# Kernel tuning notes

Hardware: AMD Instinct MI355X
Metric: run time of the kernel (lower is better)

## Reference

```python
import jax, jax.numpy as jnp
import numpy as np

N = 50000          # nodes
E = 800000         # edges (avg degree 16)
DIN = 128          # d_input
H = 8              # heads per layer
D = 16             # per-head hidden dim
HID = H * D        # 128
ALPHA = 0.2        # LeakyReLU negative slope in GAT attention
BN_EPS = 1e-5


def _xavier(key, shape):
    fan_in, fan_out = shape[0], shape[-1]
    lim = np.sqrt(6.0 / (fan_in + fan_out)).astype(np.float32)
    return jax.random.uniform(key, shape, jnp.float32, -lim, lim)


def setup_inputs() -> dict:
    key = jax.random.key(0)
    ks = jax.random.split(key, 8)
    x = jax.random.normal(ks[0], (N, DIN), jnp.float32)
    edge_idx = jax.random.randint(ks[1], (2, E), 0, N)
    W1 = _xavier(ks[2], (DIN, HID))
    a1 = _xavier(ks[3], (H, 2 * D))
    W2 = _xavier(ks[4], (HID, HID))
    a2 = _xavier(ks[5], (H, 2 * D))
    W3 = _xavier(ks[6], (HID, HID))
    a3 = _xavier(ks[7], (H, 2 * D))
    ones = jnp.ones((HID,), jnp.float32)
    zeros = jnp.zeros((HID,), jnp.float32)
    return {"x": x, "edge_idx": edge_idx,
            "W1": W1, "a1": a1, "W2": W2, "a2": a2, "W3": W3, "a3": a3,
            "g1": ones, "b1": zeros, "g2": ones, "b2": zeros, "g3": ones, "b3": zeros}


def _leaky(x):
    return jnp.where(x >= 0, x, ALPHA * x)


def _gat_layer(x, src, dst, W, a):
    # x: [N, Fin]; W: [Fin, H*D]; a: [H, 2D]
    h = (x @ W).reshape(-1, H, D)                       # [N, H, D]
    e_src = jnp.einsum('nhd,hd->nh', h, a[:, :D])       # a^T part for source node
    e_dst = jnp.einsum('nhd,hd->nh', h, a[:, D:])       # a^T part for destination node
    e = _leaky(e_src[src] + e_dst[dst])                 # [E, H]
    m = jax.ops.segment_max(e, dst, num_segments=N)     # per-dst stable softmax max
    m = jnp.where(jnp.isfinite(m), m, 0.0)              # empty segments -> 0
    w = jnp.exp(e - m[dst])                             # [E, H]
    den = jax.ops.segment_sum(w, dst, num_segments=N)   # [N, H]
    agg = jax.ops.segment_sum(h[src] * w[:, :, None], dst, num_segments=N)  # [N, H, D]
    out = agg / (den[:, :, None] + 1e-16)
    return out.reshape(-1, HID)                         # concat heads


def _bn(x, g, b):
    # BatchNorm1d training-mode math over the node axis
    mu = x.mean(axis=0)
    var = x.var(axis=0)
    return g * (x - mu) * jax.lax.rsqrt(var + BN_EPS) + b


def reference(x, edge_idx, W1, a1, W2, a2, W3, a3, g1, b1, g2, b2, g3, b3):
    src, dst = edge_idx[0], edge_idx[1]
    h1 = jax.nn.elu(_bn(_gat_layer(x, src, dst, W1, a1), g1, b1))
    h2 = jax.nn.elu(_bn(_gat_layer(h1, src, dst, W2, a2), g2, b2))
    h3_in = h1 + h2  # skip connection
    return _bn(_gat_layer(h3_in, src, dst, W3, a3), g3, b3)
```

## Files before the change

### kernel.cpp

```cpp
#include <hip/hip_runtime.h>
#include <hip/hip_bf16.h>
#include <hip/hip_fp16.h>
#include <cstddef>

#define NNODES 50000
#define NEDGES 800000
#define HID 128
#define NHEAD 8
#define AGG_NB (NNODES / 16)
#define NSLICE 64
#define SLAYER (NSLICE * 512)

#define NBUCK 196
#define BCH 2048
#define BIN_NB ((NEDGES + BCH - 1) / BCH)

typedef __attribute__((ext_vector_type(4))) float floatx4;
typedef _Float16 __attribute__((ext_vector_type(8))) half8;
typedef _Float16 __attribute__((ext_vector_type(2))) half2v;

static inline size_t align_up(size_t x, size_t a) { return (x + a - 1) & ~(a - 1); }

__device__ inline float fexp2(float x) {
#if __has_builtin(__builtin_amdgcn_exp2f)
    return __builtin_amdgcn_exp2f(x);
#else
    return __expf(x * 0.69314718055994531f);
#endif
}

__device__ inline unsigned short f2h(float f) {
    return __builtin_bit_cast(unsigned short, (_Float16)f);
}

__global__ __launch_bounds__(256) void init_kernel(const float* __restrict__ W1,
                                                   const float* __restrict__ W2,
                                                   const float* __restrict__ W3,
                                                   unsigned short* __restrict__ Wt,
                                                   int* __restrict__ zeroA, int nA,
                                                   float* __restrict__ zeroB, int nB) {
    int b = blockIdx.x;
    int t = threadIdx.x;
    if (b < 192) {
        int layer = b >> 6;
        const float* W = (layer == 0) ? W1 : ((layer == 1) ? W2 : W3);
        int idx = (b & 63) * 256 + t;
        int n = idx & 127;
        int k = idx >> 7;
        Wt[layer * 16384 + n * 128 + k] = f2h(W[idx]);
    } else {
        int nb = gridDim.x - 192;
        int bb = b - 192;
        for (int i = bb * 256 + t; i < nA; i += nb * 256) zeroA[i] = 0;
        for (int i = bb * 256 + t; i < nB; i += nb * 256) zeroB[i] = 0.f;
    }
}

__global__ __launch_bounds__(256) void bin_count_kernel(const int* __restrict__ edge,
                                                        int* __restrict__ bucketCnt) {
    __shared__ int h[NBUCK];
    int t = threadIdx.x;
    if (t < NBUCK) h[t] = 0;
    __syncthreads();
    for (int i = blockIdx.x * 256 + t; i < NEDGES; i += gridDim.x * 256)
        atomicAdd(&h[edge[NEDGES + i] >> 8], 1);
    __syncthreads();
    if (t < NBUCK && h[t]) atomicAdd(&bucketCnt[t], h[t]);
}

__global__ __launch_bounds__(256) void bucket_scan_kernel(const int* __restrict__ bucketCnt,
                                                          int* __restrict__ bucketBase) {
    __shared__ int sA[256];
    int t = threadIdx.x;
    int v = (t < NBUCK) ? bucketCnt[t] : 0;
    sA[t] = v;
    __syncthreads();
    for (int off = 1; off < 256; off <<= 1) {
        int x = (t >= off) ? sA[t - off] : 0;
        __syncthreads();
        sA[t] += x;
        __syncthreads();
    }
    if (t < NBUCK) bucketBase[t] = sA[t] - v;
    if (t == 0) bucketBase[NBUCK] = NEDGES;
}

__global__ __launch_bounds__(256) void bin_scatter_kernel(const int* __restrict__ edge,
                                                          const int* __restrict__ bucketBase,
                                                          int* __restrict__ bucketCursor,
                                                          unsigned int* __restrict__ binned) {
    __shared__ int sA[256];
    __shared__ int hcnt[NBUCK];
    __shared__ int hbase[NBUCK];
    __shared__ int gbase[NBUCK];
    __shared__ unsigned int sEnt[BCH];
    __shared__ unsigned char sBk[BCH];
    int t = threadIdx.x;
    int e0 = blockIdx.x * BCH;
    int nv = NEDGES - e0;
    if (nv > BCH) nv = BCH;

    if (t < NBUCK) hcnt[t] = 0;
    __syncthreads();

    int myB[8];
    int myR[8];
    unsigned int myP[8];
    #pragma unroll
    for (int j = 0; j < 8; ++j) {
        int idx = j * 256 + t;
        myB[j] = -1;
        if (idx < nv) {
            int s = edge[e0 + idx];
            int d = edge[NEDGES + e0 + idx];
            int bk = d >> 8;
            myB[j] = bk;
            myP[j] = (unsigned)s | ((unsigned)(d & 255) << 16);
            myR[j] = atomicAdd(&hcnt[bk], 1);
        }
    }
    __syncthreads();
    int hc = (t < NBUCK) ? hcnt[t] : 0;
    sA[t] = hc;
    __syncthreads();
    for (int off = 1; off < 256; off <<= 1) {
        int x = (t >= off) ? sA[t - off] : 0;
        __syncthreads();
        sA[t] += x;
        __syncthreads();
    }
    if (t < NBUCK) {
        hbase[t] = sA[t] - hc;
        gbase[t] = bucketBase[t] + atomicAdd(&bucketCursor[t], hc);
    }
    __syncthreads();
    #pragma unroll
    for (int j = 0; j < 8; ++j) {
        if (myB[j] >= 0) {
            int p = hbase[myB[j]] + myR[j];
            sEnt[p] = myP[j];
            sBk[p] = (unsigned char)myB[j];
        }
    }
    __syncthreads();
    #pragma unroll
    for (int j = 0; j < 8; ++j) {
        int i = j * 256 + t;
        if (i < nv) {
            int bk = sBk[i];
            binned[gbase[bk] + (i - hbase[bk])] = sEnt[i];
        }
    }
}

__global__ __launch_bounds__(256) void fine_csr_kernel(const int* __restrict__ bucketCnt,
                                                       const int* __restrict__ bucketBase,
                                                       const unsigned int* __restrict__ binned,
                                                       int* __restrict__ offs,
                                                       int* __restrict__ csr) {
    __shared__ int sA[256];
    __shared__ int sB[256];
    int t = threadIdx.x;
    int b = blockIdx.x;
    int cntb = bucketCnt[b];
    int base = bucketBase[b];
    sB[t] = 0;
    __syncthreads();
    for (int i = t; i < cntb; i += 256)
        atomicAdd(&sB[(binned[base + i] >> 16) & 255], 1);
    __syncthreads();
    int nc = sB[t];
    sA[t] = nc;
    __syncthreads();
    for (int off = 1; off < 256; off <<= 1) {
        int x = (t >= off) ? sA[t - off] : 0;
        __syncthreads();
        sA[t] += x;
        __syncthreads();
    }
    int nodeBase = base + sA[t] - nc;
    int gid = b * 256 + t;
    if (gid < NNODES) offs[gid] = nodeBase;
    if (b == NBUCK - 1 && t == 0) offs[NNODES] = NEDGES;
    sB[t] = nodeBase;
    __syncthreads();
    for (int i = t; i < cntb; i += 256) {
        unsigned e = binned[base + i];
        int pos = atomicAdd(&sB[(e >> 16) & 255], 1);
        csr[pos] = (int)(e & 0xFFFFu);
    }
}

__global__ __launch_bounds__(256) void bn_finalize_kernel(const float* __restrict__ statsPart,
                                                          const float* __restrict__ g,
                                                          const float* __restrict__ b,
                                                          float* __restrict__ ssv) {
    __shared__ float sm[256];
    int t = threadIdx.x;
    const float* base = statsPart + (t & 127) + ((t >> 7) << 7);
    float s = 0.f;
    #pragma unroll 8
    for (int k = 0; k < NSLICE; ++k) s += base[k * 512];
    sm[t] = s;
    __syncthreads();
    if (t < 128) {
        float mu = sm[t] / (float)NNODES;
        float var = sm[128 + t] / (float)NNODES - mu * mu;
        float rstd = rsqrtf(var + 1e-5f);
        float scale = g[t] * rstd;
        ssv[t] = scale;
        ssv[128 + t] = b[t] - mu * scale;
    }
}

#define GROWS 64
#define ASTRIDE 136
#define LOG2E 1.4426950408889634f
__global__ __launch_bounds__(256, 4) void gemm_kernel(const float* __restrict__ Xin,
                                                      const float* __restrict__ skip,
                                                      const float* __restrict__ ssv,
                                                      const unsigned short* __restrict__ Wt,
                                                      const float* __restrict__ a,
                                                      float* __restrict__ Hw,
                                                      unsigned short* __restrict__ Hb,
                                                      float* __restrict__ esrc,
                                                      float* __restrict__ edst,
                                                      int mode) {
    __shared__ unsigned short As[GROWS * ASTRIDE];
    int tid = threadIdx.x;
    int rowBase = blockIdx.x * GROWS;

    int r = tid >> 2;
    int cs = (tid & 3) * 32;
    int gr = rowBase + r;
    bool valid = gr < NNODES;
    float4 vv[8];
    if (valid) {
        #pragma unroll
        for (int j = 0; j < 8; ++j)
            vv[j] = *(const float4*)(Xin + (size_t)gr * HID + cs + j * 4);
    } else {
        #pragma unroll
        for (int j = 0; j < 8; ++j) vv[j] = make_float4(0.f, 0.f, 0.f, 0.f);
    }

    if (mode >= 1 && valid) {
        #pragma unroll
        for (int j = 0; j < 8; ++j) {
            int ch = cs + j * 4;
            float4 sc = *(const float4*)(ssv + ch);
            float4 sh = *(const float4*)(ssv + 128 + ch);
            float4 v = vv[j];
            v.x = sc.x * v.x + sh.x;
            v.y = sc.y * v.y + sh.y;
            v.z = sc.z * v.z + sh.z;
            v.w = sc.w * v.w + sh.w;
            v.x = (v.x > 0.f) ? v.x : expm1f(v.x);
            v.y = (v.y > 0.f) ? v.y : expm1f(v.y);
            v.z = (v.z > 0.f) ? v.z : expm1f(v.z);
            v.w = (v.w > 0.f) ? v.w : expm1f(v.w);
            if (mode == 2) {
                float4 s = *(const float4*)(skip + (size_t)gr * HID + ch);
                v.x += s.x; v.y += s.y; v.z += s.z; v.w += s.w;
            }
            vv[j] = v;
        }
        if (mode == 1) {
            #pragma unroll
            for (int j = 0; j < 8; ++j)
                *(float4*)(Hw + (size_t)gr * HID + cs + j * 4) = vv[j];
        }
    }
    {
        unsigned int pk[16];
        #pragma unroll
        for (int j = 0; j < 8; ++j) {
            pk[2 * j]     = __builtin_bit_cast(unsigned int,
                                __builtin_amdgcn_cvt_pkrtz(vv[j].x, vv[j].y));
            pk[2 * j + 1] = __builtin_bit_cast(unsigned int,
                                __builtin_amdgcn_cvt_pkrtz(vv[j].z, vv[j].w));
        }
        #pragma unroll
        for (int q = 0; q < 4; ++q)
            *(uint4*)(&As[r * ASTRIDE + cs + q * 8]) =
                make_uint4(pk[4 * q], pk[4 * q + 1], pk[4 * q + 2], pk[4 * q + 3]);
    }

    int wv = tid >> 6;
    int lane = tid & 63;
    int l15 = lane & 15;
    int quad = lane >> 4;
    const unsigned short* Arow = &As[(wv * 16 + l15) * ASTRIDE + quad * 8];
    half8 af[4];
    #pragma unroll
    for (int c = 0; c < 4; ++c) af[c] = *(const half8*)(Arow + c * 32);

    floatx4 acc[8];
    #pragma unroll
    for (int h = 0; h < 8; ++h) {
        acc[h] = (floatx4){0.f, 0.f, 0.f, 0.f};
        const unsigned short* Brow = Wt + (h * 16 + l15) * 128 + quad * 8;
        #pragma unroll
        for (int c = 0; c < 4; ++c) {
            half8 bfr = *(const half8*)(Brow + c * 32);
            acc[h] = __builtin_amdgcn_mfma_f32_16x16x32_f16(af[c], bfr, acc[h], 0, 0, 0);
        }
    }

    #pragma unroll
    for (int h = 0; h < 8; ++h) {
        #pragma unroll
        for (int reg = 0; reg < 4; ++reg)
            As[(wv * 16 + quad * 4 + reg) * ASTRIDE + h * 16 + l15] = f2h(acc[h][reg]);
    }

    {
        int rr = tid >> 2;
        int hp = tid & 3;
        int grr = rowBase + rr;
        const unsigned short* row = &As[rr * ASTRIDE + hp * 32];
        uint4 u[4];
        #pragma unroll
        for (int q = 0; q < 4; ++q) u[q] = *(const uint4*)(row + q * 8);
        if (grr < NNODES) {
            uint4* dst = (uint4*)(Hb + (size_t)grr * HID + hp * 32);
            #pragma unroll
            for (int q = 0; q < 4; ++q) dst[q] = u[q];
            float f[32];
            #pragma unroll
            for (int q = 0; q < 4; ++q) {
                unsigned int* pu = (unsigned int*)&u[q];
                #pragma unroll
                for (int j = 0; j < 4; ++j) {
                    half2v hv = __builtin_bit_cast(half2v, pu[j]);
                    f[q * 8 + 2 * j]     = (float)hv[0];
                    f[q * 8 + 2 * j + 1] = (float)hv[1];
                }
            }
            int h0 = hp * 2, h1 = hp * 2 + 1;
            float es0 = 0.f, ev0 = 0.f, es1 = 0.f, ev1 = 0.f;
            #pragma unroll
            for (int j = 0; j < 16; ++j) {
                es0 += f[j] * a[h0 * 32 + j];
                ev0 += f[j] * a[h0 * 32 + 16 + j];
                es1 += f[16 + j] * a[h1 * 32 + j];
                ev1 += f[16 + j] * a[h1 * 32 + 16 + j];
            }
            esrc[grr * NHEAD + h0] = es0 * LOG2E;
            esrc[grr * NHEAD + h1] = es1 * LOG2E;
            edst[grr * NHEAD + h0] = ev0 * LOG2E;
            edst[grr * NHEAD + h1] = ev1 * LOG2E;
        }
    }
}

__global__ __launch_bounds__(256) void aggregate_kernel(const int* __restrict__ offs,
                                                        const int* __restrict__ csr,
                                                        const float* __restrict__ esrc,
                                                        const float* __restrict__ edst,
                                                        const unsigned int* __restrict__ Hb,
                                                        float* __restrict__ out,
                                                        float* __restrict__ statsPart) {
    int tid = threadIdx.x;
    int wv = tid >> 6;
    int lane = tid & 63;
    int grp = lane >> 4;
    int sub = lane & 15;
    int head = sub >> 1;
    int n = blockIdx.x * 16 + wv * 4 + grp;
    int beg = offs[n], end = offs[n + 1];
    float ed = edst[n * NHEAD + head];
    float acc[8];
    #pragma unroll
    for (int q = 0; q < 8; ++q) acc[q] = 0.f;
    float den = 0.f;
    for (int i = beg; i < end; i += 4) {
        int ss[4];
        #pragma unroll
        for (int j = 0; j < 4; ++j)
            ss[j] = csr[min(i + j, end - 1)];
        float ee[4];
        uint4 hh[4];
        #pragma unroll
        for (int j = 0; j < 4; ++j)
            ee[j] = esrc[(unsigned)ss[j] * 8u + (unsigned)head];
        #pragma unroll
        for (int j = 0; j < 4; ++j)
            hh[j] = *(const uint4*)(Hb + (unsigned)ss[j] * 64u + (unsigned)sub * 4u);
        #pragma unroll
        for (int j = 0; j < 4; ++j) {
            float e = ee[j] + ed;
            e = fmaxf(e, 0.2f * e);
            float w = fexp2(e);
            w = (i + j < end) ? w : 0.f;
            den += w;
            half2v h0 = __builtin_bit_cast(half2v, hh[j].x);
            half2v h1 = __builtin_bit_cast(half2v, hh[j].y);
            half2v h2 = __builtin_bit_cast(half2v, hh[j].z);
            half2v h3 = __builtin_bit_cast(half2v, hh[j].w);
            acc[0] += w * (float)h0[0];
            acc[1] += w * (float)h0[1];
            acc[2] += w * (float)h1[0];
            acc[3] += w * (float)h1[1];
            acc[4] += w * (float)h2[0];
            acc[5] += w * (float)h2[1];
            acc[6] += w * (float)h3[0];
            acc[7] += w * (float)h3[1];
        }
    }
    float inv = 1.f / (den + 1e-16f);
    float4 o0 = make_float4(acc[0] * inv, acc[1] * inv, acc[2] * inv, acc[3] * inv);
    float4 o1 = make_float4(acc[4] * inv, acc[5] * inv, acc[6] * inv, acc[7] * inv);
    float* orow = out + (size_t)n * HID + sub * 8;
    *(float4*)orow = o0;
    *(float4*)(orow + 4) = o1;

    __shared__ float sm[16 * 136];
    float* srow = &sm[(wv * 4 + grp) * 136 + sub * 8];
    *(float4*)srow = o0;
    *(float4*)(srow + 4) = o1;
    __syncthreads();
    if (tid < 128) {
        float s = 0.f, s2 = 0.f;
        #pragma unroll
        for (int rr = 0; rr < 16; ++rr) {
            float v = sm[rr * 136 + tid];
            s += v;
            s2 += v * v;
        }
        float* slice = statsPart + (blockIdx.x & (NSLICE - 1)) * 512;
        atomicAdd(&slice[tid], s);
        atomicAdd(&slice[128 + tid], s2);
    }
}

__global__ __launch_bounds__(256) void final_apply_kernel(const float* __restrict__ X,
                                                          const float* __restrict__ ssv,
                                                          float* __restrict__ out) {
    __shared__ float ssm[256];
    int tid = threadIdx.x;
    ssm[tid] = ssv[tid];
    __syncthreads();
    int total4 = NNODES * HID / 4;
    for (int i = blockIdx.x * 256 + tid; i < total4; i += gridDim.x * 256) {
        float4 v = ((const float4*)X)[i];
        int c4 = (i & 31) * 4;
        float4 sc = *(const float4*)(ssm + c4);
        float4 sh = *(const float4*)(ssm + 128 + c4);
        v.x = sc.x * v.x + sh.x;
        v.y = sc.y * v.y + sh.y;
        v.z = sc.z * v.z + sh.z;
        v.w = sc.w * v.w + sh.w;
        ((float4*)out)[i] = v;
    }
}

extern "C" void kernel_launch(void* const* d_in, const int* in_sizes, int n_in,
                              void* d_out, int out_size, void* d_ws, size_t ws_size,
                              hipStream_t stream) {
    const float* x   = (const float*)d_in[0];
    const int* edge  = (const int*)d_in[1];
    const float* W1  = (const float*)d_in[2];
    const float* a1  = (const float*)d_in[3];
    const float* W2  = (const float*)d_in[4];
    const float* a2  = (const float*)d_in[5];
    const float* W3  = (const float*)d_in[6];
    const float* a3  = (const float*)d_in[7];
    const float* g1  = (const float*)d_in[8];
    const float* b1  = (const float*)d_in[9];
    const float* g2  = (const float*)d_in[10];
    const float* b2  = (const float*)d_in[11];
    const float* g3  = (const float*)d_in[12];
    const float* b3  = (const float*)d_in[13];
    float* outp      = (float*)d_out;

    char* p = (char*)d_ws;
    size_t cur = 0;
    auto carve = [&](size_t bytes) {
        void* r = p + cur;
        cur = align_up(cur + bytes, 256);
        return r;
    };
    int*   offs   = (int*)carve((NNODES + 1) * sizeof(int));
    int*   csr    = (int*)carve(NEDGES * sizeof(int));
    unsigned short* wt = (unsigned short*)carve(3 * 16384 * sizeof(unsigned short));
    unsigned short* hb = (unsigned short*)carve((size_t)NNODES * HID * sizeof(unsigned short));
    float* agg    = (float*)carve((size_t)NNODES * HID * sizeof(float));
    float* h1     = (float*)carve((size_t)NNODES * HID * sizeof(float));
    float* esrc   = (float*)carve((size_t)NNODES * NHEAD * sizeof(float));
    float* edst   = (float*)carve((size_t)NNODES * NHEAD * sizeof(float));
    float* stats  = (float*)carve(3 * SLAYER * sizeof(float));
    int*   bcnt   = (int*)carve((3 * NBUCK + 1) * sizeof(int));
    int*   bcur   = bcnt + NBUCK;
    int*   bbase  = bcnt + 2 * NBUCK;
    float* ssv    = (float*)carve(3 * 256 * sizeof(float));
    float* stats1 = stats;
    float* stats2 = stats + SLAYER;
    float* stats3 = stats + 2 * SLAYER;
    float* ssv1 = ssv;
    float* ssv2 = ssv + 256;
    float* ssv3 = ssv + 512;
    unsigned int* binned = (unsigned int*)h1;

    const int GB = (NNODES + GROWS - 1) / GROWS;

    init_kernel<<<256, 256, 0, stream>>>(W1, W2, W3, wt,
                                         bcnt, 2 * NBUCK,
                                         stats, 3 * SLAYER);
    bin_count_kernel<<<256, 256, 0, stream>>>(edge, bcnt);
    bucket_scan_kernel<<<1, 256, 0, stream>>>(bcnt, bbase);
    bin_scatter_kernel<<<BIN_NB, 256, 0, stream>>>(edge, bbase, bcur, binned);
    fine_csr_kernel<<<NBUCK, 256, 0, stream>>>(bcnt, bbase, binned, offs, csr);

    gemm_kernel<<<GB, 256, 0, stream>>>(x, nullptr, nullptr,
                                        wt, a1, nullptr, hb, esrc, edst, 0);
    aggregate_kernel<<<AGG_NB, 256, 0, stream>>>(offs, csr, esrc, edst,
                                                 (const unsigned int*)hb, agg, stats1);
    bn_finalize_kernel<<<1, 256, 0, stream>>>(stats1, g1, b1, ssv1);

    gemm_kernel<<<GB, 256, 0, stream>>>(agg, nullptr, ssv1,
                                        wt + 16384, a2, h1, hb, esrc, edst, 1);
    aggregate_kernel<<<AGG_NB, 256, 0, stream>>>(offs, csr, esrc, edst,
                                                 (const unsigned int*)hb, agg, stats2);
    bn_finalize_kernel<<<1, 256, 0, stream>>>(stats2, g2, b2, ssv2);

    gemm_kernel<<<GB, 256, 0, stream>>>(agg, h1, ssv2,
                                        wt + 32768, a3, nullptr, hb, esrc, edst, 2);
    aggregate_kernel<<<AGG_NB, 256, 0, stream>>>(offs, csr, esrc, edst,
                                                 (const unsigned int*)hb, agg, stats3);
    bn_finalize_kernel<<<1, 256, 0, stream>>>(stats3, g3, b3, ssv3);

    final_apply_kernel<<<768, 256, 0, stream>>>(agg, ssv3, outp);
}
```

Baseline: 407.1 us.

## Load GEMM A fragments directly from global and split head columns across waves

After: 395.2 us. 1.03x faster.

```diff
diff --git a/kernel.cpp b/kernel.cpp
--- a/kernel.cpp
+++ b/kernel.cpp
@@ -213,8 +213,8 @@
     }
 }
 
-#define GROWS 64
-#define ASTRIDE 136
+#define GROWS 32
+#define TSTRIDE 76
 #define LOG2E 1.4426950408889634f
 __global__ __launch_bounds__(256, 4) void gemm_kernel(const float* __restrict__ Xin,
                                                       const float* __restrict__ skip,
@@ -226,130 +226,150 @@
                                                       float* __restrict__ esrc,
                                                       float* __restrict__ edst,
                                                       int mode) {
-    __shared__ unsigned short As[GROWS * ASTRIDE];
+    __shared__ unsigned short As[4 * 16 * TSTRIDE];
     int tid = threadIdx.x;
-    int rowBase = blockIdx.x * GROWS;
-
-    int r = tid >> 2;
-    int cs = (tid & 3) * 32;
-    int gr = rowBase + r;
-    bool valid = gr < NNODES;
-    float4 vv[8];
-    if (valid) {
-        #pragma unroll
-        for (int j = 0; j < 8; ++j)
-            vv[j] = *(const float4*)(Xin + (size_t)gr * HID + cs + j * 4);
-    } else {
-        #pragma unroll
-        for (int j = 0; j < 8; ++j) vv[j] = make_float4(0.f, 0.f, 0.f, 0.f);
-    }
-
-    if (mode >= 1 && valid) {
-        #pragma unroll
-        for (int j = 0; j < 8; ++j) {
-            int ch = cs + j * 4;
-            float4 sc = *(const float4*)(ssv + ch);
-            float4 sh = *(const float4*)(ssv + 128 + ch);
-            float4 v = vv[j];
-            v.x = sc.x * v.x + sh.x;
-            v.y = sc.y * v.y + sh.y;
-            v.z = sc.z * v.z + sh.z;
-            v.w = sc.w * v.w + sh.w;
-            v.x = (v.x > 0.f) ? v.x : expm1f(v.x);
-            v.y = (v.y > 0.f) ? v.y : expm1f(v.y);
-            v.z = (v.z > 0.f) ? v.z : expm1f(v.z);
-            v.w = (v.w > 0.f) ? v.w : expm1f(v.w);
-            if (mode == 2) {
-                float4 s = *(const float4*)(skip + (size_t)gr * HID + ch);
-                v.x += s.x; v.y += s.y; v.z += s.z; v.w += s.w;
-            }
-            vv[j] = v;
-        }
-        if (mode == 1) {
-            #pragma unroll
-            for (int j = 0; j < 8; ++j)
-                *(float4*)(Hw + (size_t)gr * HID + cs + j * 4) = vv[j];
-        }
-    }
-    {
-        unsigned int pk[16];
-        #pragma unroll
-        for (int j = 0; j < 8; ++j) {
-            pk[2 * j]     = __builtin_bit_cast(unsigned int,
-                                __builtin_amdgcn_cvt_pkrtz(vv[j].x, vv[j].y));
-            pk[2 * j + 1] = __builtin_bit_cast(unsigned int,
-                                __builtin_amdgcn_cvt_pkrtz(vv[j].z, vv[j].w));
-        }
-        #pragma unroll
-        for (int q = 0; q < 4; ++q)
-            *(uint4*)(&As[r * ASTRIDE + cs + q * 8]) =
-                make_uint4(pk[4 * q], pk[4 * q + 1], pk[4 * q + 2], pk[4 * q + 3]);
-    }
-
     int wv = tid >> 6;
     int lane = tid & 63;
     int l15 = lane & 15;
     int quad = lane >> 4;
-    const unsigned short* Arow = &As[(wv * 16 + l15) * ASTRIDE + quad * 8];
+    int whalf = wv & 1;
+    int rowBase = blockIdx.x * GROWS + (wv >> 1) * 16;
+    int gr = rowBase + l15;
+    bool valid = gr < NNODES;
+
+    float4 va[8];
+    if (valid) {
+        const float* xr = Xin + (size_t)gr * HID + quad * 8;
+        #pragma unroll
+        for (int c = 0; c < 4; ++c) {
+            va[2 * c]     = *(const float4*)(xr + c * 32);
+            va[2 * c + 1] = *(const float4*)(xr + c * 32 + 4);
+        }
+    } else {
+        #pragma unroll
+        for (int j = 0; j < 8; ++j) va[j] = make_float4(0.f, 0.f, 0.f, 0.f);
+    }
+    float4 vs[8];
+    if (mode == 2 && valid) {
+        const float* sr = skip + (size_t)gr * HID + quad * 8;
+        #pragma unroll
+        for (int c = 0; c < 4; ++c) {
+            vs[2 * c]     = *(const float4*)(sr + c * 32);
+            vs[2 * c + 1] = *(const float4*)(sr + c * 32 + 4);
+        }
+    }
+
+    half8 bf[2][4];
+    {
+        const unsigned short* wb = Wt + ((whalf * 4) * 16 + l15) * 128 + quad * 8;
+        #pragma unroll
+        for (int c = 0; c < 4; ++c) bf[0][c] = *(const half8*)(wb + c * 32);
+    }
+
+    if (mode >= 1 && valid) {
+        #pragma unroll
+        for (int c = 0; c < 4; ++c) {
+            #pragma unroll
+            for (int hh = 0; hh < 2; ++hh) {
+                int ch = quad * 8 + c * 32 + hh * 4;
+                float4 sc = *(const float4*)(ssv + ch);
+                float4 sh = *(const float4*)(ssv + 128 + ch);
+                float4 v = va[2 * c + hh];
+                v.x = sc.x * v.x + sh.x;
+                v.y = sc.y * v.y + sh.y;
+                v.z = sc.z * v.z + sh.z;
+                v.w = sc.w * v.w + sh.w;
+                v.x = (v.x > 0.f) ? v.x : expm1f(v.x);
+                v.y = (v.y > 0.f) ? v.y : expm1f(v.y);
+                v.z = (v.z > 0.f) ? v.z : expm1f(v.z);
+                v.w = (v.w > 0.f) ? v.w : expm1f(v.w);
+                if (mode == 2) {
+                    float4 s = vs[2 * c + hh];
+                    v.x += s.x; v.y += s.y; v.z += s.z; v.w += s.w;
+                }
+                va[2 * c + hh] = v;
+            }
+        }
+        if (mode == 1 && whalf == 0) {
+            float* hw = Hw + (size_t)gr * HID + quad * 8;
+            #pragma unroll
+            for (int c = 0; c < 4; ++c) {
+                *(float4*)(hw + c * 32)     = va[2 * c];
+                *(float4*)(hw + c * 32 + 4) = va[2 * c + 1];
+            }
+        }
+    }
     half8 af[4];
     #pragma unroll
-    for (int c = 0; c < 4; ++c) af[c] = *(const half8*)(Arow + c * 32);
-
-    floatx4 acc[8];
-    #pragma unroll
-    for (int h = 0; h < 8; ++h) {
-        acc[h] = (floatx4){0.f, 0.f, 0.f, 0.f};
-        const unsigned short* Brow = Wt + (h * 16 + l15) * 128 + quad * 8;
-        #pragma unroll
-        for (int c = 0; c < 4; ++c) {
-            half8 bfr = *(const half8*)(Brow + c * 32);
-            acc[h] = __builtin_amdgcn_mfma_f32_16x16x32_f16(af[c], bfr, acc[h], 0, 0, 0);
-        }
-    }
-
-    #pragma unroll
-    for (int h = 0; h < 8; ++h) {
+    for (int c = 0; c < 4; ++c) {
+        uint4 pk;
+        pk.x = __builtin_bit_cast(unsigned int, __builtin_amdgcn_cvt_pkrtz(va[2*c].x,   va[2*c].y));
+        pk.y = __builtin_bit_cast(unsigned int, __builtin_amdgcn_cvt_pkrtz(va[2*c].z,   va[2*c].w));
+        pk.z = __builtin_bit_cast(unsigned int, __builtin_amdgcn_cvt_pkrtz(va[2*c+1].x, va[2*c+1].y));
+        pk.w = __builtin_bit_cast(unsigned int, __builtin_amdgcn_cvt_pkrtz(va[2*c+1].z, va[2*c+1].w));
+        af[c] = __builtin_bit_cast(half8, pk);
+    }
+
+    floatx4 acc[4];
+    #pragma unroll
+    for (int hb = 0; hb < 4; ++hb) {
+        if (hb < 3) {
+            const unsigned short* wn = Wt + ((whalf * 4 + hb + 1) * 16 + l15) * 128 + quad * 8;
+            #pragma unroll
+            for (int c = 0; c < 4; ++c) bf[(hb + 1) & 1][c] = *(const half8*)(wn + c * 32);
+        }
+        acc[hb] = (floatx4){0.f, 0.f, 0.f, 0.f};
+        #pragma unroll
+        for (int c = 0; c < 4; ++c)
+            acc[hb] = __builtin_amdgcn_mfma_f32_16x16x32_f16(af[c], bf[hb & 1][c], acc[hb], 0, 0, 0);
+    }
+
+    unsigned short* ws = &As[wv * 16 * TSTRIDE];
+    #pragma unroll
+    for (int hb = 0; hb < 4; ++hb) {
         #pragma unroll
         for (int reg = 0; reg < 4; ++reg)
-            As[(wv * 16 + quad * 4 + reg) * ASTRIDE + h * 16 + l15] = f2h(acc[h][reg]);
+            ws[(quad * 4 + reg) * TSTRIDE + hb * 16 + l15] = f2h(acc[hb][reg]);
     }
 
     {
-        int rr = tid >> 2;
-        int hp = tid & 3;
-        int grr = rowBase + rr;
-        const unsigned short* row = &As[rr * ASTRIDE + hp * 32];
-        uint4 u[4];
-        #pragma unroll
-        for (int q = 0; q < 4; ++q) u[q] = *(const uint4*)(row + q * 8);
-        if (grr < NNODES) {
-            uint4* dst = (uint4*)(Hb + (size_t)grr * HID + hp * 32);
-            #pragma unroll
-            for (int q = 0; q < 4; ++q) dst[q] = u[q];
-            float f[32];
-            #pragma unroll
-            for (int q = 0; q < 4; ++q) {
-                unsigned int* pu = (unsigned int*)&u[q];
+        int rloc = lane >> 2;
+        int cpart = lane & 3;
+        int grow = rowBase + rloc;
+        const unsigned short* rrow = &ws[rloc * TSTRIDE + cpart * 16];
+        uint4 u0 = *(const uint4*)(rrow);
+        uint4 u1 = *(const uint4*)(rrow + 8);
+        if (grow < NNODES) {
+            int chb = whalf * 64 + cpart * 16;
+            uint4* dst = (uint4*)(Hb + (size_t)grow * HID + chb);
+            dst[0] = u0;
+            dst[1] = u1;
+            float f[16];
+            {
+                unsigned int* pu = (unsigned int*)&u0;
                 #pragma unroll
                 for (int j = 0; j < 4; ++j) {
                     half2v hv = __builtin_bit_cast(half2v, pu[j]);
-                    f[q * 8 + 2 * j]     = (float)hv[0];
-                    f[q * 8 + 2 * j + 1] = (float)hv[1];
+                    f[2 * j]     = (float)hv[0];
+                    f[2 * j + 1] = (float)hv[1];
+                }
+                pu = (unsigned int*)&u1;
+                #pragma unroll
+                for (int j = 0; j < 4; ++j) {
+                    half2v hv = __builtin_bit_cast(half2v, pu[j]);
+                    f[8 + 2 * j]     = (float)hv[0];
+                    f[8 + 2 * j + 1] = (float)hv[1];
                 }
             }
-            int h0 = hp * 2, h1 = hp * 2 + 1;
-            float es0 = 0.f, ev0 = 0.f, es1 = 0.f, ev1 = 0.f;
+            int head = whalf * 4 + cpart;
+            float es = 0.f, ev = 0.f;
             #pragma unroll
             for (int j = 0; j < 16; ++j) {
-                es0 += f[j] * a[h0 * 32 + j];
-                ev0 += f[j] * a[h0 * 32 + 16 + j];
-                es1 += f[16 + j] * a[h1 * 32 + j];
-                ev1 += f[16 + j] * a[h1 * 32 + 16 + j];
+                es += f[j] * a[head * 32 + j];
+                ev += f[j] * a[head * 32 + 16 + j];
             }
-            esrc[grr * NHEAD + h0] = es0 * LOG2E;
-            esrc[grr * NHEAD + h1] = es1 * LOG2E;
-            edst[grr * NHEAD + h0] = ev0 * LOG2E;
-            edst[grr * NHEAD + h1] = ev1 * LOG2E;
+            esrc[grow * NHEAD + head] = es * LOG2E;
+            edst[grow * NHEAD + head] = ev * LOG2E;
         }
     }
 }
```

## Stage GEMM weights in LDS and keep the h1 skip activation in fp16

Applied to the files above, without the earlier changes.

Measured after the change: 373.4 us. 1.09x faster.

```diff
diff --git a/kernel.cpp b/kernel.cpp
--- a/kernel.cpp
+++ b/kernel.cpp
@@ -216,19 +216,27 @@
 #define GROWS 64
 #define ASTRIDE 136
 #define LOG2E 1.4426950408889634f
-__global__ __launch_bounds__(256, 4) void gemm_kernel(const float* __restrict__ Xin,
-                                                      const float* __restrict__ skip,
-                                                      const float* __restrict__ ssv,
-                                                      const unsigned short* __restrict__ Wt,
-                                                      const float* __restrict__ a,
-                                                      float* __restrict__ Hw,
-                                                      unsigned short* __restrict__ Hb,
-                                                      float* __restrict__ esrc,
-                                                      float* __restrict__ edst,
-                                                      int mode) {
+__global__ __launch_bounds__(256) void gemm_kernel(const float* __restrict__ Xin,
+                                                   const unsigned short* __restrict__ skip16,
+                                                   const float* __restrict__ ssv,
+                                                   const unsigned short* __restrict__ Wt,
+                                                   const float* __restrict__ a,
+                                                   unsigned short* __restrict__ Hw16,
+                                                   unsigned short* __restrict__ Hb,
+                                                   float* __restrict__ esrc,
+                                                   float* __restrict__ edst,
+                                                   int mode) {
     __shared__ unsigned short As[GROWS * ASTRIDE];
+    __shared__ unsigned short Bs[128 * ASTRIDE];
     int tid = threadIdx.x;
     int rowBase = blockIdx.x * GROWS;
+
+    uint4 breg[8];
+    #pragma unroll
+    for (int q = 0; q < 8; ++q) {
+        int i = q * 256 + tid;
+        breg[q] = *(const uint4*)(Wt + (i >> 4) * 128 + (i & 15) * 8);
+    }
 
     int r = tid >> 2;
     int cs = (tid & 3) * 32;
@@ -244,7 +252,19 @@
         for (int j = 0; j < 8; ++j) vv[j] = make_float4(0.f, 0.f, 0.f, 0.f);
     }
 
+    #pragma unroll
+    for (int q = 0; q < 8; ++q) {
+        int i = q * 256 + tid;
+        *(uint4*)(&Bs[(i >> 4) * ASTRIDE + (i & 15) * 8]) = breg[q];
+    }
+
     if (mode >= 1 && valid) {
+        uint4 sk[4];
+        if (mode == 2) {
+            #pragma unroll
+            for (int q = 0; q < 4; ++q)
+                sk[q] = *(const uint4*)(skip16 + (size_t)gr * HID + cs + q * 8);
+        }
         #pragma unroll
         for (int j = 0; j < 8; ++j) {
             int ch = cs + j * 4;
@@ -260,15 +280,15 @@
             v.z = (v.z > 0.f) ? v.z : expm1f(v.z);
             v.w = (v.w > 0.f) ? v.w : expm1f(v.w);
             if (mode == 2) {
-                float4 s = *(const float4*)(skip + (size_t)gr * HID + ch);
-                v.x += s.x; v.y += s.y; v.z += s.z; v.w += s.w;
+                const unsigned int* pu = (const unsigned int*)&sk[j >> 1];
+                half2v s0 = __builtin_bit_cast(half2v, pu[(j & 1) * 2]);
+                half2v s1 = __builtin_bit_cast(half2v, pu[(j & 1) * 2 + 1]);
+                v.x += (float)s0[0];
+                v.y += (float)s0[1];
+                v.z += (float)s1[0];
+                v.w += (float)s1[1];
             }
             vv[j] = v;
-        }
-        if (mode == 1) {
-            #pragma unroll
-            for (int j = 0; j < 8; ++j)
-                *(float4*)(Hw + (size_t)gr * HID + cs + j * 4) = vv[j];
         }
     }
     {
@@ -280,11 +300,19 @@
             pk[2 * j + 1] = __builtin_bit_cast(unsigned int,
                                 __builtin_amdgcn_cvt_pkrtz(vv[j].z, vv[j].w));
         }
+        if (mode == 1 && valid) {
+            #pragma unroll
+            for (int q = 0; q < 4; ++q)
+                *(uint4*)(Hw16 + (size_t)gr * HID + cs + q * 8) =
+                    make_uint4(pk[4 * q], pk[4 * q + 1], pk[4 * q + 2], pk[4 * q + 3]);
+        }
         #pragma unroll
         for (int q = 0; q < 4; ++q)
             *(uint4*)(&As[r * ASTRIDE + cs + q * 8]) =
                 make_uint4(pk[4 * q], pk[4 * q + 1], pk[4 * q + 2], pk[4 * q + 3]);
     }
+
+    __syncthreads();
 
     int wv = tid >> 6;
     int lane = tid & 63;
@@ -299,7 +327,7 @@
     #pragma unroll
     for (int h = 0; h < 8; ++h) {
         acc[h] = (floatx4){0.f, 0.f, 0.f, 0.f};
-        const unsigned short* Brow = Wt + (h * 16 + l15) * 128 + quad * 8;
+        const unsigned short* Brow = &Bs[(h * 16 + l15) * ASTRIDE + quad * 8];
         #pragma unroll
         for (int c = 0; c < 4; ++c) {
             half8 bfr = *(const half8*)(Brow + c * 32);
@@ -486,7 +514,7 @@
     unsigned short* wt = (unsigned short*)carve(3 * 16384 * sizeof(unsigned short));
     unsigned short* hb = (unsigned short*)carve((size_t)NNODES * HID * sizeof(unsigned short));
     float* agg    = (float*)carve((size_t)NNODES * HID * sizeof(float));
-    float* h1     = (float*)carve((size_t)NNODES * HID * sizeof(float));
+    unsigned short* h1 = (unsigned short*)carve((size_t)NNODES * HID * sizeof(unsigned short));
     float* esrc   = (float*)carve((size_t)NNODES * NHEAD * sizeof(float));
     float* edst   = (float*)carve((size_t)NNODES * NHEAD * sizeof(float));
     float* stats  = (float*)carve(3 * SLAYER * sizeof(float));
```
